# Optimization experiments

Hardware: AMD Instinct MI355X
Metric: run time of the kernel (lower is better)

## Reference

```python
import jax, jax.numpy as jnp
import numpy as np

B, L, D, H = 2, 2048, 1024, 16
HD = D // H  # head_dim = 64


def setup_inputs() -> dict:
    key = jax.random.key(0)
    ks = jax.random.split(key, 6)
    return {
        "q": jax.random.normal(ks[0], (B, L, D), dtype=jnp.float32),
        "k": jax.random.normal(ks[1], (B, L, D), dtype=jnp.float32),
        "v": jax.random.normal(ks[2], (B, L, D), dtype=jnp.float32),
        "Wq": jax.random.normal(ks[3], (D, D), dtype=jnp.float32) * (D ** -0.5),
        "Wk": jax.random.normal(ks[4], (D, D), dtype=jnp.float32) * (D ** -0.5),
        "Wv": jax.random.normal(ks[5], (D, D), dtype=jnp.float32) * (D ** -0.5),
    }


def reference(q, k, v, Wq, Wk, Wv):
    # nn.Linear(bias=False): y = x @ W.T ; then split heads -> [B,H,L,HD]
    def proj(x, W):
        return (x @ W.T).reshape(B, L, H, HD).transpose(0, 2, 1, 3)

    Q = proj(q, Wq)
    K = proj(k, Wk)
    V = proj(v, Wv)
    scale = HD ** -0.5
    idx = jnp.arange(L)
    # flex_attention score_mod: score + (q_idx - kv_idx), applied after scaling
    bias = (idx[:, None] - idx[None, :]).astype(q.dtype)  # [L, L]
    scores = jnp.einsum('bhqd,bhkd->bhqk', Q, K) * scale + bias
    attn = jax.nn.softmax(scores, axis=-1)
    out = jnp.einsum('bhqk,bhkd->bhqd', attn, V)
    # 'b h l d -> b l (h d)'
    return out.transpose(0, 2, 1, 3).reshape(B, L, D)
```

## Files before the change

### kernel.cpp

```cpp
#include <hip/hip_runtime.h>

#define DEVFN __device__ __forceinline__

typedef __attribute__((ext_vector_type(8))) short bf16x8;
typedef __attribute__((ext_vector_type(4))) float f32x4;

constexpr int cB = 2, cL = 2048, cD = 1024, cH = 16, cHD = 64;
constexpr int KWIN  = 128;
constexpr int SLICE = 262144;

#if __has_builtin(__builtin_amdgcn_exp2f)
#define EXP2F(x) __builtin_amdgcn_exp2f(x)
#else
#define EXP2F(x) __expf(0.6931471805599453f * (x))
#endif

DEVFN unsigned short hu(float f) {
  return (unsigned short)((__float_as_uint(f) + 0x8000u) >> 16);
}
DEVFN unsigned pkhu(float a, float b) {
  unsigned ua = __float_as_uint(a) + 0x8000u;
  unsigned ub = __float_as_uint(b) + 0x8000u;
  return __builtin_amdgcn_perm(ub, ua, 0x07060302u);
}
DEVFN uint4 pk8(float4 a, float4 b) {
  return (uint4){pkhu(a.x, a.y), pkhu(a.z, a.w), pkhu(b.x, b.y), pkhu(b.z, b.w)};
}

#if __has_builtin(__builtin_amdgcn_global_load_lds)
#define HAVE_ASYNC 1
typedef const __attribute__((address_space(1))) unsigned int* gas1_t;
typedef __attribute__((address_space(3))) unsigned int* las3_t;
#define ASYNC_CP16(g, l) \
  __builtin_amdgcn_global_load_lds((gas1_t)(g), (las3_t)(l), 16, 0, 0)
#else
#define HAVE_ASYNC 0
#endif

DEVFN int swzofs(int row, int cc) { return row * 64 + (((cc) ^ (row & 7)) << 3); }

__global__ __launch_bounds__(256)
void proj_kv(const float* __restrict__ kf, const float* __restrict__ vf,
             const float* __restrict__ Wkf, const float* __restrict__ Wvf,
             unsigned short* __restrict__ Kc, unsigned short* __restrict__ Vc) {
  __shared__ __align__(16) unsigned short As[128 * 64];
  __shared__ __align__(16) unsigned short Bs[64 * 64];
  const int tid = threadIdx.x;
  const int wv = tid >> 6, lane = tid & 63, id = lane & 15, quad = lane >> 4;
  const int wr = wv >> 1, wc = wv & 1;
  const int rl = lane >> 3, cc = (lane & 7) ^ rl;

  const int bx = blockIdx.x;
  int mode, M0, N0;
  const float *A, *B;
  unsigned short* outp;
  if (bx < 32) {
    mode = 1; A = kf; B = Wkf; outp = Kc;
    M0 = (bx & 1) * KWIN;
    N0 = (bx >> 1) * 64;
  } else {
    const int t = bx - 32;
    mode = 2; A = Wvf; B = vf; outp = Vc;
    M0 = (t & 7) * 128;
    const int y = t >> 3;
    N0 = (y >> 1) * KWIN + (y & 1) * 64;
  }
  const bool aslice = (mode == 1);

  f32x4 acc[4][2];
#pragma unroll
  for (int i = 0; i < 4; ++i)
#pragma unroll
    for (int j = 0; j < 2; ++j) acc[i][j] = (f32x4){0.f, 0.f, 0.f, 0.f};

  for (int k0 = 0; k0 < cD; k0 += 64) {
    float4 ra[4][2], rb[2][2];
#pragma unroll
    for (int c = 0; c < 4; ++c) {
      const int r = M0 + c * 32 + wv * 8 + rl;
      const size_t grow = aslice ? ((size_t)(r >> 7) * cL + (r & 127)) : (size_t)r;
      const float* p = A + grow * cD + k0 + cc * 8;
      ra[c][0] = *(const float4*)p;
      ra[c][1] = *(const float4*)(p + 4);
    }
#pragma unroll
    for (int c = 0; c < 2; ++c) {
      const int r = N0 + c * 32 + wv * 8 + rl;
      const size_t grow = aslice ? (size_t)r : ((size_t)(r >> 7) * cL + (r & 127));
      const float* p = B + grow * cD + k0 + cc * 8;
      rb[c][0] = *(const float4*)p;
      rb[c][1] = *(const float4*)(p + 4);
    }
    __syncthreads();
#pragma unroll
    for (int c = 0; c < 4; ++c)
      *(uint4*)&As[(c * 32 + wv * 8) * 64 + lane * 8] = pk8(ra[c][0], ra[c][1]);
#pragma unroll
    for (int c = 0; c < 2; ++c)
      *(uint4*)&Bs[(c * 32 + wv * 8) * 64 + lane * 8] = pk8(rb[c][0], rb[c][1]);
    __syncthreads();

#pragma unroll
    for (int ks = 0; ks < 2; ++ks) {
      bf16x8 af[4], bfr[2];
#pragma unroll
      for (int mi = 0; mi < 4; ++mi)
        af[mi] = *(const bf16x8*)&As[swzofs(wr * 64 + mi * 16 + id, ks * 4 + quad)];
#pragma unroll
      for (int ni = 0; ni < 2; ++ni)
        bfr[ni] = *(const bf16x8*)&Bs[swzofs(wc * 32 + ni * 16 + id, ks * 4 + quad)];
#pragma unroll
      for (int mi = 0; mi < 4; ++mi)
#pragma unroll
        for (int ni = 0; ni < 2; ++ni)
          acc[mi][ni] = __builtin_amdgcn_mfma_f32_16x16x32_bf16(
              af[mi], bfr[ni], acc[mi][ni], 0, 0, 0);
    }
  }

#pragma unroll
  for (int mi = 0; mi < 4; ++mi) {
#pragma unroll
    for (int ni = 0; ni < 2; ++ni) {
#pragma unroll
      for (int rg = 0; rg < 4; ++rg) {
        const int mr = M0 + wr * 64 + mi * 16 + quad * 4 + rg;
        const int nc = N0 + wc * 32 + ni * 16 + id;
        size_t idx;
        if (mode == 1) {
          const int b = mr >> 7, l = mr & 127, h = nc >> 6, hd = nc & 63;
          idx = ((size_t)((b * cH + h) * KWIN + l)) * cHD + hd;
        } else {
          const int h = mr >> 6, hd = mr & 63, b = nc >> 7, l = nc & 127;
          idx = ((size_t)((b * cH + h) * cHD + hd)) * KWIN + l;
        }
        outp[idx] = hu(acc[mi][ni][rg]);
      }
    }
  }
}

__global__ __launch_bounds__(512, 4)
void fused_qattn(const float* __restrict__ Xq,
                 const float* __restrict__ Wqf,
                 const unsigned short* __restrict__ Kc,
                 const unsigned short* __restrict__ Vc,
                 float* __restrict__ out) {
  __shared__ __align__(16) unsigned short lds[40960];
  unsigned short* Ks = lds + 24576;
  unsigned short* Vs = lds + 32768;
  unsigned short* Ps = lds + 16384;

  const int tid = threadIdx.x;
  const int wv = tid >> 6, lane = tid & 63, id = lane & 15, quad = lane >> 4;
  const int wr = wv >> 1, wc = wv & 1;
  const int rl = lane >> 3, cc = (lane & 7) ^ rl;
  const int bh = blockIdx.y, q0 = blockIdx.x * 128;
  const int bb = bh >> 4, h = bh & 15;
  const size_t M0 = (size_t)bb * cL + q0;
  const float* Bw = Wqf + (size_t)(h * cHD) * cD;
  const unsigned short* Kb = Kc + (size_t)bh * KWIN * cHD;
  const unsigned short* Vb = Vc + (size_t)bh * cHD * KWIN;

  const int rbase = wv * 8;

#if HAVE_ASYNC
#pragma unroll
  for (int c = 0; c < 2; ++c)
    ASYNC_CP16(Kb + (size_t)(c * 64 + rbase + rl) * cHD + cc * 8,
               &Ks[(c * 64 + rbase) * 64]);
#pragma unroll
  for (int it = 0; it < 2; ++it)
    ASYNC_CP16(Vb + (size_t)(rbase + rl) * KWIN + it * 64 + cc * 8,
               &Vs[it * 4096 + rbase * 64]);
#else
  {
    uint4 kv0r = *(const uint4*)(Kb + (size_t)(rbase + rl) * cHD + cc * 8);
    uint4 kv1r = *(const uint4*)(Kb + (size_t)(64 + rbase + rl) * cHD + cc * 8);
    uint4 vv0r = *(const uint4*)(Vb + (size_t)(rbase + rl) * KWIN + cc * 8);
    uint4 vv1r = *(const uint4*)(Vb + (size_t)(rbase + rl) * KWIN + 64 + cc * 8);
    *(uint4*)&Ks[rbase * 64 + lane * 8] = kv0r;
    *(uint4*)&Ks[(64 + rbase) * 64 + lane * 8] = kv1r;
    *(uint4*)&Vs[rbase * 64 + lane * 8] = vv0r;
    *(uint4*)&Vs[4096 + rbase * 64 + lane * 8] = vv1r;
  }
#endif

  float4 sA[2][2], sB[2];
#define STAGE_LOAD(k0)                                                         \
  {                                                                            \
    _Pragma("unroll")                                                          \
    for (int c = 0; c < 2; ++c) {                                              \
      const float* p_ = Xq + (M0 + c * 64 + wv * 8 + rl) * cD + (k0) + cc * 8; \
      sA[c][0] = *(const float4*)p_;                                           \
      sA[c][1] = *(const float4*)(p_ + 4);                                     \
    }                                                                          \
    {                                                                          \
      const float* p_ = Bw + (size_t)(wv * 8 + rl) * cD + (k0) + cc * 8;       \
      sB[0] = *(const float4*)p_;                                              \
      sB[1] = *(const float4*)(p_ + 4);                                        \
    }                                                                          \
  }
#define STAGE_WRITE(buf)                                                       \
  {                                                                            \
    unsigned short* A_ = lds + (buf) * 8192;                                   \
    unsigned short* B_ = lds + 16384 + (buf) * 4096;                           \
    _Pragma("unroll")                                                          \
    for (int c = 0; c < 2; ++c)                                                \
      *(uint4*)&A_[(c * 64 + wv * 8) * 64 + lane * 8] = pk8(sA[c][0], sA[c][1]); \
    *(uint4*)&B_[(wv * 8) * 64 + lane * 8] = pk8(sB[0], sB[1]);                \
  }

  f32x4 acc[2][2];
#pragma unroll
  for (int i = 0; i < 2; ++i)
#pragma unroll
    for (int j = 0; j < 2; ++j) acc[i][j] = (f32x4){0.f, 0.f, 0.f, 0.f};

  STAGE_LOAD(0);
  STAGE_WRITE(0);
  __syncthreads();

#pragma unroll
  for (int t = 0; t < 16; ++t) {
    const int cur = t & 1;
    if (t < 15) STAGE_LOAD((t + 1) * 64);

    const unsigned short* A_ = lds + cur * 8192;
    const unsigned short* B_ = lds + 16384 + cur * 4096;
#pragma unroll
    for (int ks = 0; ks < 2; ++ks) {
      bf16x8 af[2], bfr[2];
#pragma unroll
      for (int mi = 0; mi < 2; ++mi)
        af[mi] = *(const bf16x8*)&A_[swzofs(wr * 32 + mi * 16 + id, ks * 4 + quad)];
#pragma unroll
      for (int ni = 0; ni < 2; ++ni)
        bfr[ni] = *(const bf16x8*)&B_[swzofs(wc * 32 + ni * 16 + id, ks * 4 + quad)];
#pragma unroll
      for (int mi = 0; mi < 2; ++mi)
#pragma unroll
        for (int ni = 0; ni < 2; ++ni)
          acc[mi][ni] = __builtin_amdgcn_mfma_f32_16x16x32_bf16(
              af[mi], bfr[ni], acc[mi][ni], 0, 0, 0);
    }
    if (t < 15) STAGE_WRITE(cur ^ 1);
    __syncthreads();
  }

#pragma unroll
  for (int mi = 0; mi < 2; ++mi)
#pragma unroll
    for (int ni = 0; ni < 2; ++ni)
#pragma unroll
      for (int rg = 0; rg < 4; ++rg) {
        const int qrow = wr * 32 + mi * 16 + quad * 4 + rg;
        const int col  = wc * 32 + ni * 16 + id;
        lds[swzofs(qrow, col >> 3) + (col & 7)] = hu(acc[mi][ni][rg]);
      }
  __syncthreads();

  bf16x8 aq[2];
#pragma unroll
  for (int ks = 0; ks < 2; ++ks)
    aq[ks] = *(const bf16x8*)&lds[swzofs(wv * 16 + id, ks * 4 + quad)];

  constexpr float L2E = 1.4426950408889634f;
  constexpr float SC2 = 0.125f * L2E;

  f32x4 oacc[4];
#pragma unroll
  for (int i = 0; i < 4; ++i) oacc[i] = (f32x4){0.f, 0.f, 0.f, 0.f};
  float m_i[4], l_i[4];
#pragma unroll
  for (int i = 0; i < 4; ++i) { m_i[i] = -1e30f; l_i[i] = 0.f; }

  for (int it = 0; it < 2; ++it) {
    const int kv0 = it * 64;

    f32x4 sa[4];
#pragma unroll
    for (int nt = 0; nt < 4; ++nt) sa[nt] = (f32x4){0.f, 0.f, 0.f, 0.f};
#pragma unroll
    for (int ks = 0; ks < 2; ++ks)
#pragma unroll
      for (int nt = 0; nt < 4; ++nt) {
        bf16x8 kf = *(const bf16x8*)&Ks[swzofs(kv0 + nt * 16 + id, ks * 4 + quad)];
        sa[nt] = __builtin_amdgcn_mfma_f32_16x16x32_bf16(aq[ks], kf, sa[nt], 0, 0, 0);
      }

    const float tkv = (float)(kv0 + id) * L2E;
    float negkb[4];
#pragma unroll
    for (int nt = 0; nt < 4; ++nt) negkb[nt] = -(tkv + (float)(nt * 16) * L2E);

    float z[4][4], mt[4];
#pragma unroll
    for (int i = 0; i < 4; ++i) {
#pragma unroll
      for (int nt = 0; nt < 4; ++nt)
        z[i][nt] = fmaf(sa[nt][i], SC2, negkb[nt]);
      mt[i] = fmaxf(fmaxf(z[i][0], z[i][1]), fmaxf(z[i][2], z[i][3]));
    }
#pragma unroll
    for (int mk = 1; mk < 16; mk <<= 1)
#pragma unroll
      for (int i = 0; i < 4; ++i)
        mt[i] = fmaxf(mt[i], __shfl_xor(mt[i], mk));

    float p[4][4], rs[4], al[4];
#pragma unroll
    for (int i = 0; i < 4; ++i) {
      const float mn = fmaxf(m_i[i], mt[i]);
      al[i] = EXP2F(m_i[i] - mn);
      m_i[i] = mn;
      float s = 0.f;
#pragma unroll
      for (int nt = 0; nt < 4; ++nt) { p[i][nt] = EXP2F(z[i][nt] - mn); s += p[i][nt]; }
      rs[i] = s;
    }
#pragma unroll
    for (int mk = 1; mk < 16; mk <<= 1)
#pragma unroll
      for (int i = 0; i < 4; ++i) rs[i] += __shfl_xor(rs[i], mk);
#pragma unroll
    for (int i = 0; i < 4; ++i) l_i[i] = l_i[i] * al[i] + rs[i];
#pragma unroll
    for (int nh = 0; nh < 4; ++nh)
#pragma unroll
      for (int i = 0; i < 4; ++i) oacc[nh][i] *= al[i];

#pragma unroll
    for (int i = 0; i < 4; ++i) {
      const int qrow = wv * 16 + quad * 4 + i;
#pragma unroll
      for (int nt = 0; nt < 4; ++nt) {
        const int col = nt * 16 + id;
        Ps[swzofs(qrow, col >> 3) + (col & 7)] = hu(p[i][nt]);
      }
    }

    bf16x8 pf[2];
#pragma unroll
    for (int ks2 = 0; ks2 < 2; ++ks2)
      pf[ks2] = *(const bf16x8*)&Ps[swzofs(wv * 16 + id, ks2 * 4 + quad)];
#pragma unroll
    for (int ks2 = 0; ks2 < 2; ++ks2)
#pragma unroll
      for (int nh = 0; nh < 4; ++nh) {
        bf16x8 vf = *(const bf16x8*)&Vs[it * 4096 + swzofs(nh * 16 + id, ks2 * 4 + quad)];
        oacc[nh] = __builtin_amdgcn_mfma_f32_16x16x32_bf16(pf[ks2], vf, oacc[nh], 0, 0, 0);
      }
  }

#pragma unroll
  for (int i = 0; i < 4; ++i) {
    const float inv = 1.0f / l_i[i];
    const int qrow = q0 + wv * 16 + quad * 4 + i;
    float* op = out + ((size_t)(bb * cL + qrow)) * cD + h * cHD + id;
#pragma unroll
    for (int nh = 0; nh < 4; ++nh)
      op[nh * 16] = oacc[nh][i] * inv;
  }
}

extern "C" void kernel_launch(void* const* d_in, const int* in_sizes, int n_in,
                              void* d_out, int out_size, void* d_ws, size_t ws_size,
                              hipStream_t stream) {
  const float* q  = (const float*)d_in[0];
  const float* k  = (const float*)d_in[1];
  const float* v  = (const float*)d_in[2];
  const float* Wq = (const float*)d_in[3];
  const float* Wk = (const float*)d_in[4];
  const float* Wv = (const float*)d_in[5];
  float* out = (float*)d_out;

  unsigned short* Kc = (unsigned short*)d_ws;
  unsigned short* Vc = Kc + SLICE;

  proj_kv<<<dim3(64), dim3(256), 0, stream>>>(k, v, Wk, Wv, Kc, Vc);
  fused_qattn<<<dim3(16, 32), dim3(512), 0, stream>>>(q, Wq, Kc, Vc, out);
}
```

Baseline: 149.3 us.

## Pre-convert Q and Wq to bf16, load A fragments directly from global

Adds a conversion kernel that writes q and Wq as bf16 into the workspace, so the fused kernel no longer reads fp32 and packs it for every block. In the fused kernel each wave now owns 16 query rows and loads its A fragments straight from global memory into registers. Only the Wq tile is staged through LDS, using async global-to-LDS copies, which shrinks LDS use and drops the min-blocks launch bound. The cost is an extra launch plus a round trip of the bf16 copies through memory. Each B tile in LDS is also reread by all waves.

```diff
diff --git a/kernel.cpp b/kernel.cpp
--- a/kernel.cpp
+++ b/kernel.cpp
@@ -6,6 +6,8 @@
 typedef __attribute__((ext_vector_type(4))) float f32x4;
 
 constexpr int cB = 2, cL = 2048, cD = 1024, cH = 16, cHD = 64;
+constexpr int ELE   = 4194304;
+constexpr int WELE  = 1048576;
 constexpr int KWIN  = 128;
 constexpr int SLICE = 262144;
 
@@ -38,6 +40,20 @@
 #endif
 
 DEVFN int swzofs(int row, int cc) { return row * 64 + (((cc) ^ (row & 7)) << 3); }
+
+__global__ __launch_bounds__(256)
+void conv_bf16(const float* __restrict__ q, const float* __restrict__ Wq,
+               unsigned short* __restrict__ qb, unsigned short* __restrict__ wqb) {
+  const int y = blockIdx.y;
+  const int i8 = (blockIdx.x * 256 + threadIdx.x) * 8;
+  const float* src = (y == 0) ? q : Wq;
+  unsigned short* dst = (y == 0) ? qb : wqb;
+  const int n = (y == 0) ? ELE : WELE;
+  if (i8 >= n) return;
+  float4 a = *(const float4*)(src + i8);
+  float4 b4 = *(const float4*)(src + i8 + 4);
+  *(uint4*)(dst + i8) = pk8(a, b4);
+}
 
 __global__ __launch_bounds__(256)
 void proj_kv(const float* __restrict__ kf, const float* __restrict__ vf,
@@ -140,25 +156,25 @@
   }
 }
 
-__global__ __launch_bounds__(512, 4)
-void fused_qattn(const float* __restrict__ Xq,
-                 const float* __restrict__ Wqf,
+__global__ __launch_bounds__(512)
+void fused_qattn(const unsigned short* __restrict__ Qb,
+                 const unsigned short* __restrict__ Wqb,
                  const unsigned short* __restrict__ Kc,
                  const unsigned short* __restrict__ Vc,
                  float* __restrict__ out) {
-  __shared__ __align__(16) unsigned short lds[40960];
-  unsigned short* Ks = lds + 24576;
-  unsigned short* Vs = lds + 32768;
-  unsigned short* Ps = lds + 16384;
+  __shared__ __align__(16) unsigned short lds[24576];
+  unsigned short* Ks = lds + 8192;
+  unsigned short* Vs = lds + 16384;
+  unsigned short* Ps = lds;
 
   const int tid = threadIdx.x;
   const int wv = tid >> 6, lane = tid & 63, id = lane & 15, quad = lane >> 4;
-  const int wr = wv >> 1, wc = wv & 1;
   const int rl = lane >> 3, cc = (lane & 7) ^ rl;
   const int bh = blockIdx.y, q0 = blockIdx.x * 128;
   const int bb = bh >> 4, h = bh & 15;
-  const size_t M0 = (size_t)bb * cL + q0;
-  const float* Bw = Wqf + (size_t)(h * cHD) * cD;
+  const unsigned short* Arow =
+      Qb + (size_t)(bb * cL + q0 + wv * 16 + id) * cD;
+  const unsigned short* Bw = Wqb + (size_t)(h * cHD) * cD;
   const unsigned short* Kb = Kc + (size_t)bh * KWIN * cHD;
   const unsigned short* Vb = Vc + (size_t)bh * cHD * KWIN;
 
@@ -186,84 +202,61 @@
   }
 #endif
 
-  float4 sA[2][2], sB[2];
-#define STAGE_LOAD(k0)                                                         \
+#if HAVE_ASYNC
+#define STAGE_B(buf, k0)                                                       \
+  ASYNC_CP16(Bw + (size_t)(wv * 8 + rl) * cD + (k0) + cc * 8,                  \
+             &lds[(buf) * 4096 + (wv * 8) * 64]);
+#else
+#define STAGE_B(buf, k0)                                                       \
   {                                                                            \
-    _Pragma("unroll")                                                          \
-    for (int c = 0; c < 2; ++c) {                                              \
-      const float* p_ = Xq + (M0 + c * 64 + wv * 8 + rl) * cD + (k0) + cc * 8; \
-      sA[c][0] = *(const float4*)p_;                                           \
-      sA[c][1] = *(const float4*)(p_ + 4);                                     \
-    }                                                                          \
-    {                                                                          \
-      const float* p_ = Bw + (size_t)(wv * 8 + rl) * cD + (k0) + cc * 8;       \
-      sB[0] = *(const float4*)p_;                                              \
-      sB[1] = *(const float4*)(p_ + 4);                                        \
-    }                                                                          \
-  }
-#define STAGE_WRITE(buf)                                                       \
-  {                                                                            \
-    unsigned short* A_ = lds + (buf) * 8192;                                   \
-    unsigned short* B_ = lds + 16384 + (buf) * 4096;                           \
-    _Pragma("unroll")                                                          \
-    for (int c = 0; c < 2; ++c)                                                \
-      *(uint4*)&A_[(c * 64 + wv * 8) * 64 + lane * 8] = pk8(sA[c][0], sA[c][1]); \
-    *(uint4*)&B_[(wv * 8) * 64 + lane * 8] = pk8(sB[0], sB[1]);                \
-  }
-
-  f32x4 acc[2][2];
-#pragma unroll
-  for (int i = 0; i < 2; ++i)
-#pragma unroll
-    for (int j = 0; j < 2; ++j) acc[i][j] = (f32x4){0.f, 0.f, 0.f, 0.f};
-
-  STAGE_LOAD(0);
-  STAGE_WRITE(0);
+    uint4 rb_ = *(const uint4*)(Bw + (size_t)(wv * 8 + rl) * cD + (k0) + cc * 8); \
+    *(uint4*)&lds[(buf) * 4096 + (wv * 8) * 64 + lane * 8] = rb_;              \
+  }
+#endif
+
+  f32x4 acc[4];
+#pragma unroll
+  for (int i = 0; i < 4; ++i) acc[i] = (f32x4){0.f, 0.f, 0.f, 0.f};
+
+  bf16x8 afr[2][2];
+#pragma unroll
+  for (int ks = 0; ks < 2; ++ks)
+    afr[0][ks] = *(const bf16x8*)(Arow + 0 * 64 + ks * 32 + quad * 8);
+  STAGE_B(0, 0);
   __syncthreads();
 
 #pragma unroll
   for (int t = 0; t < 16; ++t) {
     const int cur = t & 1;
-    if (t < 15) STAGE_LOAD((t + 1) * 64);
-
-    const unsigned short* A_ = lds + cur * 8192;
-    const unsigned short* B_ = lds + 16384 + cur * 4096;
+    if (t < 15) {
+      STAGE_B(cur ^ 1, (t + 1) * 64);
+#pragma unroll
+      for (int ks = 0; ks < 2; ++ks)
+        afr[cur ^ 1][ks] = *(const bf16x8*)(Arow + (t + 1) * 64 + ks * 32 + quad * 8);
+    }
 #pragma unroll
     for (int ks = 0; ks < 2; ++ks) {
-      bf16x8 af[2], bfr[2];
-#pragma unroll
-      for (int mi = 0; mi < 2; ++mi)
-        af[mi] = *(const bf16x8*)&A_[swzofs(wr * 32 + mi * 16 + id, ks * 4 + quad)];
-#pragma unroll
-      for (int ni = 0; ni < 2; ++ni)
-        bfr[ni] = *(const bf16x8*)&B_[swzofs(wc * 32 + ni * 16 + id, ks * 4 + quad)];
-#pragma unroll
-      for (int mi = 0; mi < 2; ++mi)
-#pragma unroll
-        for (int ni = 0; ni < 2; ++ni)
-          acc[mi][ni] = __builtin_amdgcn_mfma_f32_16x16x32_bf16(
-              af[mi], bfr[ni], acc[mi][ni], 0, 0, 0);
-    }
-    if (t < 15) STAGE_WRITE(cur ^ 1);
+#pragma unroll
+      for (int nt = 0; nt < 4; ++nt) {
+        bf16x8 bfr = *(const bf16x8*)&lds[cur * 4096 + swzofs(nt * 16 + id, ks * 4 + quad)];
+        acc[nt] = __builtin_amdgcn_mfma_f32_16x16x32_bf16(afr[cur][ks], bfr, acc[nt], 0, 0, 0);
+      }
+    }
     __syncthreads();
   }
 
 #pragma unroll
-  for (int mi = 0; mi < 2; ++mi)
-#pragma unroll
-    for (int ni = 0; ni < 2; ++ni)
-#pragma unroll
-      for (int rg = 0; rg < 4; ++rg) {
-        const int qrow = wr * 32 + mi * 16 + quad * 4 + rg;
-        const int col  = wc * 32 + ni * 16 + id;
-        lds[swzofs(qrow, col >> 3) + (col & 7)] = hu(acc[mi][ni][rg]);
-      }
-  __syncthreads();
-
+  for (int nt = 0; nt < 4; ++nt)
+#pragma unroll
+    for (int rg = 0; rg < 4; ++rg) {
+      const int qrow = wv * 16 + quad * 4 + rg;
+      const int col  = nt * 16 + id;
+      Ps[swzofs(qrow, col >> 3) + (col & 7)] = hu(acc[nt][rg]);
+    }
   bf16x8 aq[2];
 #pragma unroll
   for (int ks = 0; ks < 2; ++ks)
-    aq[ks] = *(const bf16x8*)&lds[swzofs(wv * 16 + id, ks * 4 + quad)];
+    aq[ks] = *(const bf16x8*)&Ps[swzofs(wv * 16 + id, ks * 4 + quad)];
 
   constexpr float L2E = 1.4426950408889634f;
   constexpr float SC2 = 0.125f * L2E;
@@ -375,9 +368,12 @@
   const float* Wv = (const float*)d_in[5];
   float* out = (float*)d_out;
 
-  unsigned short* Kc = (unsigned short*)d_ws;
-  unsigned short* Vc = Kc + SLICE;
-
+  unsigned short* Qb  = (unsigned short*)d_ws;
+  unsigned short* Wqb = Qb + ELE;
+  unsigned short* Kc  = Wqb + WELE;
+  unsigned short* Vc  = Kc + SLICE;
+
+  conv_bf16<<<dim3(2048, 2), dim3(256), 0, stream>>>(q, Wq, Qb, Wqb);
   proj_kv<<<dim3(64), dim3(256), 0, stream>>>(k, v, Wk, Wv, Kc, Vc);
-  fused_qattn<<<dim3(16, 32), dim3(512), 0, stream>>>(q, Wq, Kc, Vc, out);
-}
+  fused_qattn<<<dim3(16, 32), dim3(512), 0, stream>>>(Qb, Wqb, Kc, Vc, out);
+}
```

Result: faster. 145.2 us (-2.7%).
